# Kernel optimization log

Measured on AMD Instinct MI355X. Metric: run time of the kernel, lower is better.

The kernel has to match this reference:

```python
import jax, jax.numpy as jnp
import numpy as np


def setup_inputs() -> dict:
    key = jax.random.key(0)
    T, B, I, M = 256, 64, 512, 512
    ks = jax.random.split(key, 16)
    kai_i = np.sqrt(2.0 / I)   # kaiming_normal_ fan_in
    kai_m = np.sqrt(2.0 / M)
    return {
        "inputs":   jax.random.normal(ks[0], (T, B, I), jnp.float32),
        "sememe_c": jax.random.normal(ks[1], (T, B, M), jnp.float32),
        "sememe_h": jax.random.normal(ks[2], (T, B, M), jnp.float32),
        "c0":       jax.random.normal(ks[3], (B, M), jnp.float32),
        "h0":       jax.random.normal(ks[4], (B, M), jnp.float32),
        "W_ioux": jax.random.normal(ks[5], (3 * M, I), jnp.float32) * kai_i,
        "b_ioux": jnp.zeros((3 * M,), jnp.float32),
        "W_iouh": jax.random.normal(ks[6], (3 * M, M), jnp.float32) * kai_m,
        "b_iouh": jnp.zeros((3 * M,), jnp.float32),
        "W_ious": jax.random.normal(ks[7], (3 * M, M), jnp.float32) * kai_m,
        "b_ious": jnp.zeros((3 * M,), jnp.float32),
        "W_fx":  jax.random.normal(ks[8],  (M, I), jnp.float32) * kai_i,
        "b_fx":  jnp.zeros((M,), jnp.float32),
        "W_fxs": jax.random.normal(ks[9],  (M, I), jnp.float32) * kai_i,
        "b_fxs": jnp.zeros((M,), jnp.float32),
        "W_fh":  jax.random.normal(ks[10], (M, M), jnp.float32) * kai_m,
        "b_fh":  jnp.zeros((M,), jnp.float32),
        "W_fs":  jax.random.normal(ks[11], (M, M), jnp.float32) * kai_m,
        "b_fs":  jnp.zeros((M,), jnp.float32),
    }


def reference(inputs, sememe_c, sememe_h, c0, h0,
              W_ioux, b_ioux, W_iouh, b_iouh, W_ious, b_ious,
              W_fx, b_fx, W_fxs, b_fxs, W_fh, b_fh, W_fs, b_fs):
    # Precompute all input-side projections with big GEMMs over [T*B, I].
    iou_x = jnp.einsum('tbi,oi->tbo', inputs, W_ioux) + b_ioux   # [T,B,3M]
    fx_all = jnp.einsum('tbi,oi->tbo', inputs, W_fx) + b_fx       # [T,B,M]
    fxs_all = jnp.einsum('tbi,oi->tbo', inputs, W_fxs) + b_fxs    # [T,B,M]

    def step(carry, xs):
        c, h = carry
        iou_x_t, fx_t, fxs_t, sc_t, sh_t = xs
        iou = iou_x_t + h @ W_iouh.T + b_iouh + sh_t @ W_ious.T + b_ious
        i, o, u = jnp.split(iou, 3, axis=1)
        i = jax.nn.sigmoid(i)
        o = jax.nn.sigmoid(o)
        u = jnp.tanh(u)
        f = jax.nn.sigmoid(h @ W_fh.T + b_fh + fx_t)
        f_s = jax.nn.sigmoid(sh_t @ W_fs.T + b_fs + fxs_t)
        c_new = i * u + f * c + f_s * sc_t
        h_new = o * jnp.tanh(c_new)
        return (c_new, h_new), h_new

    (c_T, h_T), output = jax.lax.scan(
        step, (c0, h0), (iou_x, fx_all, fxs_all, sememe_c, sememe_h))
    return output, c_T, h_T
```

## Files before the change

### kernel.cpp

```cpp
#include <hip/hip_runtime.h>
#include <cstdint>
#include <cstddef>


typedef _Float16 half8 __attribute__((ext_vector_type(8)));
typedef _Float16 half4 __attribute__((ext_vector_type(4)));
typedef float    f32x4 __attribute__((ext_vector_type(4)));

#define T_STEPS 256
#define B_DIM   64
#define M_DIM   512
#define KA      1024
#define NA      2560
#define MA      16384
#define NWG_REC 64
#define FLAG_STRIDE 32

__device__ __forceinline__ float sigmoidf_fast(float x) {
    return 1.0f / (1.0f + __expf(-x));
}
__device__ __forceinline__ float tanhf_fast(float x) {
    float e = __expf(2.0f * x);
    return 1.0f - 2.0f / (e + 1.0f);
}


__global__ void conv_xs(const float* __restrict__ inp, const float* __restrict__ sh,
                        _Float16* __restrict__ xs) {
    int idx = blockIdx.x * blockDim.x + threadIdx.x;
    const int total = MA * KA / 8;
    if (idx >= total) return;
    int row = idx >> 7;
    int col = (idx & 127) * 8;
    const float* src = (col < 512) ? (inp + (size_t)row * 512 + col)
                                   : (sh  + (size_t)row * 512 + (col - 512));
    f32x4 a = *(const f32x4*)src;
    f32x4 b = *(const f32x4*)(src + 4);
    half8 o;
    o[0]=(_Float16)a[0]; o[1]=(_Float16)a[1]; o[2]=(_Float16)a[2]; o[3]=(_Float16)a[3];
    o[4]=(_Float16)b[0]; o[5]=(_Float16)b[1]; o[6]=(_Float16)b[2]; o[7]=(_Float16)b[3];
    *(half8*)(xs + (size_t)idx * 8) = o;
}

__global__ void conv_w(const float* __restrict__ W_ioux, const float* __restrict__ W_ious,
                       const float* __restrict__ W_fx,   const float* __restrict__ W_fxs,
                       const float* __restrict__ W_fs,   _Float16* __restrict__ wc) {
    int idx = blockIdx.x * blockDim.x + threadIdx.x;
    const int total = NA * KA / 8;
    if (idx >= total) return;
    int n = idx >> 7;
    int col = (idx & 127) * 8;
    const float* src = nullptr;
    if (col < 512) {
        int k = col;
        src = (n < 1536) ? (W_ioux + (size_t)n * 512 + k)
            : (n < 2048) ? (W_fx   + (size_t)(n - 1536) * 512 + k)
                         : (W_fxs  + (size_t)(n - 2048) * 512 + k);
    } else {
        int k = col - 512;
        if (n < 1536)      src = W_ious + (size_t)n * 512 + k;
        else if (n >= 2048) src = W_fs  + (size_t)(n - 2048) * 512 + k;
    }
    half8 o;
    if (src) {
        f32x4 a = *(const f32x4*)src;
        f32x4 b = *(const f32x4*)(src + 4);
        o[0]=(_Float16)a[0]; o[1]=(_Float16)a[1]; o[2]=(_Float16)a[2]; o[3]=(_Float16)a[3];
        o[4]=(_Float16)b[0]; o[5]=(_Float16)b[1]; o[6]=(_Float16)b[2]; o[7]=(_Float16)b[3];
    } else {
        #pragma unroll
        for (int i = 0; i < 8; ++i) o[i] = (_Float16)0.0f;
    }
    *(half8*)(wc + (size_t)idx * 8) = o;
}

__global__ void conv_wr(const float* __restrict__ W_iouh, const float* __restrict__ W_fh,
                        _Float16* __restrict__ wr) {
    int idx = blockIdx.x * blockDim.x + threadIdx.x;
    const int total = 2048 * 512 / 8;
    if (idx >= total) return;
    int n = idx >> 6;
    int col = (idx & 63) * 8;
    int wgs = n >> 5, loc = n & 31;
    int g = (loc >> 4) * 2 + ((loc >> 3) & 1);
    int m = wgs * 8 + (loc & 7);
    const float* src = (g < 3) ? (W_iouh + ((size_t)(g * 512 + m)) * 512 + col)
                               : (W_fh   + (size_t)m * 512 + col);
    f32x4 a = *(const f32x4*)src;
    f32x4 b = *(const f32x4*)(src + 4);
    half8 o;
    o[0]=(_Float16)a[0]; o[1]=(_Float16)a[1]; o[2]=(_Float16)a[2]; o[3]=(_Float16)a[3];
    o[4]=(_Float16)b[0]; o[5]=(_Float16)b[1]; o[6]=(_Float16)b[2]; o[7]=(_Float16)b[3];
    *(half8*)(wr + (size_t)idx * 8) = o;
}

__global__ void conv_h0(const float* __restrict__ h0, _Float16* __restrict__ hb) {
    int idx = blockIdx.x * blockDim.x + threadIdx.x;
    const int total = B_DIM * M_DIM / 8;
    if (idx >= total) return;
    f32x4 a = *(const f32x4*)(h0 + (size_t)idx * 8);
    f32x4 b = *(const f32x4*)(h0 + (size_t)idx * 8 + 4);
    half8 o;
    o[0]=(_Float16)a[0]; o[1]=(_Float16)a[1]; o[2]=(_Float16)a[2]; o[3]=(_Float16)a[3];
    o[4]=(_Float16)b[0]; o[5]=(_Float16)b[1]; o[6]=(_Float16)b[2]; o[7]=(_Float16)b[3];
    *(half8*)(hb + (size_t)idx * 8) = o;
}


__global__ __launch_bounds__(256, 2)
void gemm_pre(const _Float16* __restrict__ A, const _Float16* __restrict__ W,
              const float* __restrict__ b_ioux, const float* __restrict__ b_iouh,
              const float* __restrict__ b_ious, const float* __restrict__ b_fx,
              const float* __restrict__ b_fh,   const float* __restrict__ b_fxs,
              const float* __restrict__ b_fs,   const float* __restrict__ smc,
              _Float16* __restrict__ pre, _Float16* __restrict__ addc) {
    __shared__ _Float16 As[128 * 64];
    __shared__ _Float16 Bs[128 * 64];

    const int nwg = 2560;
    int orig = blockIdx.x;
    int wgid = (orig & 7) * (nwg >> 3) + (orig >> 3);
    const int bx = wgid & 127;
    const int by = wgid >> 7;
    const int m0 = bx * 128, n0 = by * 128;

    const int tid = threadIdx.x;
    const int wv = tid >> 6, lane = tid & 63;
    const int lr = lane & 15, lq = lane >> 4;
    const int wr = wv >> 1, wc = wv & 1;

    f32x4 acc[4][4];
    #pragma unroll
    for (int i = 0; i < 4; ++i)
        #pragma unroll
        for (int j = 0; j < 4; ++j)
            #pragma unroll
            for (int r = 0; r < 4; ++r) acc[i][j][r] = 0.0f;

    for (int kt = 0; kt < KA / 64; ++kt) {
        const int k0 = kt * 64;
        #pragma unroll
        for (int j = 0; j < 4; ++j) {
            int L = j * 4096 + wv * 1024 + lane * 16;
            int row = L >> 7;
            int colb = (L & 127) ^ ((row & 7) << 4);
            const char* ga = (const char*)(A + (size_t)(m0 + row) * KA + k0) + colb;
            __builtin_amdgcn_global_load_lds(
                (const __attribute__((address_space(1))) void*)ga,
                (__attribute__((address_space(3))) void*)((char*)As + j * 4096 + wv * 1024),
                16, 0, 0);
            const char* gb = (const char*)(W + (size_t)(n0 + row) * KA + k0) + colb;
            __builtin_amdgcn_global_load_lds(
                (const __attribute__((address_space(1))) void*)gb,
                (__attribute__((address_space(3))) void*)((char*)Bs + j * 4096 + wv * 1024),
                16, 0, 0);
        }
        __syncthreads();

        half8 af[4][2], bf[4][2];
        #pragma unroll
        for (int f = 0; f < 4; ++f) {
            #pragma unroll
            for (int kk = 0; kk < 2; ++kk) {
                {
                    int row = wr * 64 + f * 16 + lr;
                    int byt = row * 128 + (((kk * 32 + lq * 8) * 2) ^ ((row & 7) << 4));
                    af[f][kk] = *(const half8*)((const char*)As + byt);
                }
                {
                    int row = wc * 64 + f * 16 + lr;
                    int byt = row * 128 + (((kk * 32 + lq * 8) * 2) ^ ((row & 7) << 4));
                    bf[f][kk] = *(const half8*)((const char*)Bs + byt);
                }
            }
        }
        #pragma unroll
        for (int kk = 0; kk < 2; ++kk)
            #pragma unroll
            for (int fi = 0; fi < 4; ++fi)
                #pragma unroll
                for (int fj = 0; fj < 4; ++fj)
                    acc[fi][fj] = __builtin_amdgcn_mfma_f32_16x16x32_f16(
                        af[fi][kk], bf[fj][kk], acc[fi][fj], 0, 0, 0);
        __syncthreads();
    }

    #pragma unroll
    for (int fi = 0; fi < 4; ++fi) {
        int row0 = m0 + wr * 64 + fi * 16 + lq * 4;
        int tt = row0 >> 6;
        int b  = row0 & 63;
        #pragma unroll
        for (int fj = 0; fj < 4; ++fj) {
            int col = n0 + wc * 64 + fj * 16 + lr;
            f32x4 v = acc[fi][fj];
            if (col < 2048) {
                int g, mm; float bias;
                if (col < 1536) { g = col >> 9; mm = col & 511;
                                  bias = b_ioux[col] + b_iouh[col] + b_ious[col]; }
                else            { g = 3; mm = col - 1536; bias = b_fx[mm] + b_fh[mm]; }
                half4 hv;
                #pragma unroll
                for (int r = 0; r < 4; ++r) hv[r] = (_Float16)(v[r] + bias);
                *(half4*)(pre + ((((size_t)tt * 4 + g) * 512 + mm) * 64 + b)) = hv;
            } else {
                int mm = col - 2048;
                float bias = b_fxs[mm] + b_fs[mm];
                half4 hv;
                #pragma unroll
                for (int r = 0; r < 4; ++r) {
                    float s  = sigmoidf_fast(v[r] + bias);
                    float sc = smc[((size_t)(tt * 64 + b + r)) * 512 + mm];
                    hv[r] = (_Float16)(s * sc);
                }
                *(half4*)(addc + (((size_t)tt * 512 + mm) * 64 + b)) = hv;
            }
        }
    }
}


__global__ __launch_bounds__(256, 1)
void lstm_rec(const _Float16* __restrict__ Wr, const _Float16* __restrict__ pre,
              const _Float16* __restrict__ addc, const float* __restrict__ c0,
              _Float16* __restrict__ hbuf, float* __restrict__ out,
              int* __restrict__ flags) {
    const int wg = blockIdx.x;
    const int tid = threadIdx.x;
    const int wv = tid >> 6, lane = tid & 63;
    const int lr = lane & 15, lq = lane >> 4;
    const int c8 = (lane >> 3) & 1;
    const int m  = wg * 8 + (lane & 7);
    const int b0 = wv * 16 + lq * 4;

    half8 bfr[2][16];
    #pragma unroll
    for (int nt = 0; nt < 2; ++nt)
        #pragma unroll
        for (int kk = 0; kk < 16; ++kk)
            bfr[nt][kk] = *(const half8*)(Wr + ((size_t)(wg * 32 + nt * 16 + lr)) * 512
                                          + kk * 32 + lq * 8);

    float c[4];
    #pragma unroll
    for (int r = 0; r < 4; ++r) c[r] = c0[(size_t)(b0 + r) * 512 + m];

    half4 pv[2], av;
    #pragma unroll
    for (int nt = 0; nt < 2; ++nt) {
        int g = nt * 2 + c8;
        pv[nt] = *(const half4*)(pre + (((size_t)0 * 4 + g) * 512 + m) * 64 + b0);
    }
    av = *(const half4*)(addc + ((size_t)0 * 512 + m) * 64 + b0);

    const int* myflag = flags + lane * FLAG_STRIDE;

    for (int t = 0; t < T_STEPS; ++t) {
        const _Float16* hr = hbuf + (size_t)(t & 1) * B_DIM * M_DIM;
        const _Float16* bp = hr + (size_t)(wv * 16 + lr) * 512 + lq * 8;

        f32x4 acc[2];
        #pragma unroll
        for (int nt = 0; nt < 2; ++nt)
            #pragma unroll
            for (int r = 0; r < 4; ++r) acc[nt][r] = (float)pv[nt][r];
        half4 avc = av;

        if (t + 1 < T_STEPS) {
            #pragma unroll
            for (int nt = 0; nt < 2; ++nt) {
                int g = nt * 2 + c8;
                pv[nt] = *(const half4*)(pre + (((size_t)(t + 1) * 4 + g) * 512 + m) * 64 + b0);
            }
            av = *(const half4*)(addc + ((size_t)(t + 1) * 512 + m) * 64 + b0);
        }

        half8 af[16];
        asm volatile(
            "global_load_dwordx4 %0,  %16, off sc0 sc1\n\t"
            "global_load_dwordx4 %1,  %16, off offset:64 sc0 sc1\n\t"
            "global_load_dwordx4 %2,  %16, off offset:128 sc0 sc1\n\t"
            "global_load_dwordx4 %3,  %16, off offset:192 sc0 sc1\n\t"
            "global_load_dwordx4 %4,  %16, off offset:256 sc0 sc1\n\t"
            "global_load_dwordx4 %5,  %16, off offset:320 sc0 sc1\n\t"
            "global_load_dwordx4 %6,  %16, off offset:384 sc0 sc1\n\t"
            "global_load_dwordx4 %7,  %16, off offset:448 sc0 sc1\n\t"
            "global_load_dwordx4 %8,  %16, off offset:512 sc0 sc1\n\t"
            "global_load_dwordx4 %9,  %16, off offset:576 sc0 sc1\n\t"
            "global_load_dwordx4 %10, %16, off offset:640 sc0 sc1\n\t"
            "global_load_dwordx4 %11, %16, off offset:704 sc0 sc1\n\t"
            "global_load_dwordx4 %12, %16, off offset:768 sc0 sc1\n\t"
            "global_load_dwordx4 %13, %16, off offset:832 sc0 sc1\n\t"
            "global_load_dwordx4 %14, %16, off offset:896 sc0 sc1\n\t"
            "global_load_dwordx4 %15, %16, off offset:960 sc0 sc1\n\t"
            "s_waitcnt vmcnt(0)"
            : "=&v"(af[0]),  "=&v"(af[1]),  "=&v"(af[2]),  "=&v"(af[3]),
              "=&v"(af[4]),  "=&v"(af[5]),  "=&v"(af[6]),  "=&v"(af[7]),
              "=&v"(af[8]),  "=&v"(af[9]),  "=&v"(af[10]), "=&v"(af[11]),
              "=&v"(af[12]), "=&v"(af[13]), "=&v"(af[14]), "=&v"(af[15])
            : "v"(bp)
            : "memory");

        #pragma unroll
        for (int kk = 0; kk < 16; ++kk) {
            acc[0] = __builtin_amdgcn_mfma_f32_16x16x32_f16(af[kk], bfr[0][kk], acc[0], 0, 0, 0);
            acc[1] = __builtin_amdgcn_mfma_f32_16x16x32_f16(af[kk], bfr[1][kk], acc[1], 0, 0, 0);
        }

        float hnew[4];
        #pragma unroll
        for (int r = 0; r < 4; ++r) {
            float raw0 = acc[0][r];
            float raw1 = acc[1][r];
            float s0 = sigmoidf_fast(raw0);
            float v1 = c8 ? sigmoidf_fast(raw1) : tanhf_fast(raw1);
            float sf = __shfl_xor(v1, 8);
            float cn = s0 * v1 + sf * c[r] + (float)avc[r];
            float tc = tanhf_fast(cn);
            float tcx = __shfl_xor(tc, 8);
            if (!c8) c[r] = cn;
            hnew[r] = s0 * tcx;
        }

        if (t == T_STEPS - 1) {
            if (c8) {
                #pragma unroll
                for (int r = 0; r < 4; ++r)
                    out[((size_t)t * B_DIM + b0 + r) * M_DIM + m] = hnew[r];
            }
            size_t base = (size_t)T_STEPS * B_DIM * M_DIM;
            if (!c8) {
                #pragma unroll
                for (int r = 0; r < 4; ++r)
                    out[base + (size_t)(b0 + r) * M_DIM + m] = c[r];
            } else {
                #pragma unroll
                for (int r = 0; r < 4; ++r)
                    out[base + (size_t)B_DIM * M_DIM + (size_t)(b0 + r) * M_DIM + m] = hnew[r];
            }
        } else {
            _Float16* hw = hbuf + (size_t)((t + 1) & 1) * B_DIM * M_DIM;
            if (c8) {
                #pragma unroll
                for (int r = 0; r < 4; ++r) {
                    _Float16 hv = (_Float16)hnew[r];
                    unsigned int u = (unsigned int)__builtin_bit_cast(unsigned short, hv);
                    asm volatile("global_store_short %0, %1, off sc0 sc1"
                                 :: "v"(hw + (size_t)(b0 + r) * M_DIM + m), "v"(u)
                                 : "memory");
                }
            }
            asm volatile("s_waitcnt vmcnt(0)" ::: "memory");
            __syncthreads();
            if (tid == 0) {
                unsigned int fv = (unsigned int)(t + 1);
                asm volatile("global_store_dword %0, %1, off sc0 sc1"
                             :: "v"(flags + wg * FLAG_STRIDE), "v"(fv) : "memory");
            }
            if (c8) {
                #pragma unroll
                for (int r = 0; r < 4; ++r)
                    out[((size_t)t * B_DIM + b0 + r) * M_DIM + m] = hnew[r];
            }
            const int target = t + 1;
            while (true) {
                int v;
                asm volatile("global_load_dword %0, %1, off sc0 sc1\n\t"
                             "s_waitcnt vmcnt(0)"
                             : "=v"(v) : "v"(myflag) : "memory");
                if (__all(v >= target)) break;
                __builtin_amdgcn_s_sleep(1);
            }
        }
    }
}


extern "C" void kernel_launch(void* const* d_in, const int* in_sizes, int n_in,
                              void* d_out, int out_size, void* d_ws, size_t ws_size,
                              hipStream_t stream) {
    const float* inputs  = (const float*)d_in[0];
    const float* smc     = (const float*)d_in[1];
    const float* smh     = (const float*)d_in[2];
    const float* c0      = (const float*)d_in[3];
    const float* h0      = (const float*)d_in[4];
    const float* W_ioux  = (const float*)d_in[5];
    const float* b_ioux  = (const float*)d_in[6];
    const float* W_iouh  = (const float*)d_in[7];
    const float* b_iouh  = (const float*)d_in[8];
    const float* W_ious  = (const float*)d_in[9];
    const float* b_ious  = (const float*)d_in[10];
    const float* W_fx    = (const float*)d_in[11];
    const float* b_fx    = (const float*)d_in[12];
    const float* W_fxs   = (const float*)d_in[13];
    const float* b_fxs   = (const float*)d_in[14];
    const float* W_fh    = (const float*)d_in[15];
    const float* b_fh    = (const float*)d_in[16];
    const float* W_fs    = (const float*)d_in[17];
    const float* b_fs    = (const float*)d_in[18];

    char* ws = (char*)d_ws;
    size_t off = 0;
    auto alloc = [&](size_t bytes) {
        char* p = ws + off;
        off = (off + bytes + 255) & ~(size_t)255;
        return p;
    };
    _Float16* XS   = (_Float16*)alloc((size_t)MA * KA * 2);
    _Float16* Wc   = (_Float16*)alloc((size_t)NA * KA * 2);
    _Float16* Wr   = (_Float16*)alloc((size_t)2048 * 512 * 2);
    _Float16* hb   = (_Float16*)alloc((size_t)2 * B_DIM * M_DIM * 2);
    _Float16* pre  = (_Float16*)alloc((size_t)T_STEPS * 4 * 512 * 64 * 2);
    _Float16* addc = (_Float16*)alloc((size_t)T_STEPS * 512 * 64 * 2);
    int* flags     = (int*)alloc(NWG_REC * FLAG_STRIDE * sizeof(int));
    if (off > ws_size) return;

    hipMemsetAsync(flags, 0, NWG_REC * FLAG_STRIDE * sizeof(int), stream);
    conv_xs <<<MA * KA / 8 / 256, 256, 0, stream>>>(inputs, smh, XS);
    conv_w  <<<NA * KA / 8 / 256, 256, 0, stream>>>(W_ioux, W_ious, W_fx, W_fxs, W_fs, Wc);
    conv_wr <<<2048 * 512 / 8 / 256, 256, 0, stream>>>(W_iouh, W_fh, Wr);
    conv_h0 <<<B_DIM * M_DIM / 8 / 256, 256, 0, stream>>>(h0, hb);
    gemm_pre<<<2560, 256, 0, stream>>>(XS, Wc, b_ioux, b_iouh, b_ious, b_fx, b_fh,
                                       b_fxs, b_fs, smc, pre, addc);
    lstm_rec<<<NWG_REC, 256, 0, stream>>>(Wr, pre, addc, c0, hb, (float*)d_out, flags);
}
```

Measured before the change: 1.325 ms.

## Replace per-step flag barrier with step-tagged h values polled directly

```diff
diff --git a/kernel.cpp b/kernel.cpp
--- a/kernel.cpp
+++ b/kernel.cpp
@@ -6,6 +6,7 @@
 typedef _Float16 half8 __attribute__((ext_vector_type(8)));
 typedef _Float16 half4 __attribute__((ext_vector_type(4)));
 typedef float    f32x4 __attribute__((ext_vector_type(4)));
+typedef unsigned int uint32x4 __attribute__((ext_vector_type(4)));
 
 #define T_STEPS 256
 #define B_DIM   64
@@ -14,7 +15,6 @@
 #define NA      2560
 #define MA      16384
 #define NWG_REC 64
-#define FLAG_STRIDE 32
 
 __device__ __forceinline__ float sigmoidf_fast(float x) {
     return 1.0f / (1.0f + __expf(-x));
@@ -94,16 +94,21 @@
     *(half8*)(wr + (size_t)idx * 8) = o;
 }
 
-__global__ void conv_h0(const float* __restrict__ h0, _Float16* __restrict__ hb) {
+__global__ void conv_h0(const float* __restrict__ h0, unsigned* __restrict__ hb) {
     int idx = blockIdx.x * blockDim.x + threadIdx.x;
     const int total = B_DIM * M_DIM / 8;
     if (idx >= total) return;
     f32x4 a = *(const f32x4*)(h0 + (size_t)idx * 8);
     f32x4 b = *(const f32x4*)(h0 + (size_t)idx * 8 + 4);
-    half8 o;
-    o[0]=(_Float16)a[0]; o[1]=(_Float16)a[1]; o[2]=(_Float16)a[2]; o[3]=(_Float16)a[3];
-    o[4]=(_Float16)b[0]; o[5]=(_Float16)b[1]; o[6]=(_Float16)b[2]; o[7]=(_Float16)b[3];
-    *(half8*)(hb + (size_t)idx * 8) = o;
+    uint32x4 o0, o1;
+    #pragma unroll
+    for (int j = 0; j < 4; ++j) {
+        _Float16 ha = (_Float16)a[j], hb16 = (_Float16)b[j];
+        o0[j] = (unsigned)__builtin_bit_cast(unsigned short, ha);
+        o1[j] = (unsigned)__builtin_bit_cast(unsigned short, hb16);
+    }
+    *(uint32x4*)(hb + (size_t)idx * 8)     = o0;
+    *(uint32x4*)(hb + (size_t)idx * 8 + 4) = o1;
 }
 
 
@@ -220,11 +225,74 @@
 }
 
 
+template<int HALF>
+__device__ __forceinline__ void gather_half(const char* bp, unsigned tagv,
+                                            uint32x4 (&gv)[16]) {
+    while (true) {
+        if constexpr (HALF == 0) {
+            asm volatile(
+                "global_load_dwordx4 %0,  %16, off sc0 sc1\n\t"
+                "global_load_dwordx4 %1,  %16, off offset:16 sc0 sc1\n\t"
+                "global_load_dwordx4 %2,  %16, off offset:128 sc0 sc1\n\t"
+                "global_load_dwordx4 %3,  %16, off offset:144 sc0 sc1\n\t"
+                "global_load_dwordx4 %4,  %16, off offset:256 sc0 sc1\n\t"
+                "global_load_dwordx4 %5,  %16, off offset:272 sc0 sc1\n\t"
+                "global_load_dwordx4 %6,  %16, off offset:384 sc0 sc1\n\t"
+                "global_load_dwordx4 %7,  %16, off offset:400 sc0 sc1\n\t"
+                "global_load_dwordx4 %8,  %16, off offset:512 sc0 sc1\n\t"
+                "global_load_dwordx4 %9,  %16, off offset:528 sc0 sc1\n\t"
+                "global_load_dwordx4 %10, %16, off offset:640 sc0 sc1\n\t"
+                "global_load_dwordx4 %11, %16, off offset:656 sc0 sc1\n\t"
+                "global_load_dwordx4 %12, %16, off offset:768 sc0 sc1\n\t"
+                "global_load_dwordx4 %13, %16, off offset:784 sc0 sc1\n\t"
+                "global_load_dwordx4 %14, %16, off offset:896 sc0 sc1\n\t"
+                "global_load_dwordx4 %15, %16, off offset:912 sc0 sc1\n\t"
+                "s_waitcnt vmcnt(0)"
+                : "=&v"(gv[0]),  "=&v"(gv[1]),  "=&v"(gv[2]),  "=&v"(gv[3]),
+                  "=&v"(gv[4]),  "=&v"(gv[5]),  "=&v"(gv[6]),  "=&v"(gv[7]),
+                  "=&v"(gv[8]),  "=&v"(gv[9]),  "=&v"(gv[10]), "=&v"(gv[11]),
+                  "=&v"(gv[12]), "=&v"(gv[13]), "=&v"(gv[14]), "=&v"(gv[15])
+                : "v"(bp) : "memory");
+        } else {
+            asm volatile(
+                "global_load_dwordx4 %0,  %16, off offset:1024 sc0 sc1\n\t"
+                "global_load_dwordx4 %1,  %16, off offset:1040 sc0 sc1\n\t"
+                "global_load_dwordx4 %2,  %16, off offset:1152 sc0 sc1\n\t"
+                "global_load_dwordx4 %3,  %16, off offset:1168 sc0 sc1\n\t"
+                "global_load_dwordx4 %4,  %16, off offset:1280 sc0 sc1\n\t"
+                "global_load_dwordx4 %5,  %16, off offset:1296 sc0 sc1\n\t"
+                "global_load_dwordx4 %6,  %16, off offset:1408 sc0 sc1\n\t"
+                "global_load_dwordx4 %7,  %16, off offset:1424 sc0 sc1\n\t"
+                "global_load_dwordx4 %8,  %16, off offset:1536 sc0 sc1\n\t"
+                "global_load_dwordx4 %9,  %16, off offset:1552 sc0 sc1\n\t"
+                "global_load_dwordx4 %10, %16, off offset:1664 sc0 sc1\n\t"
+                "global_load_dwordx4 %11, %16, off offset:1680 sc0 sc1\n\t"
+                "global_load_dwordx4 %12, %16, off offset:1792 sc0 sc1\n\t"
+                "global_load_dwordx4 %13, %16, off offset:1808 sc0 sc1\n\t"
+                "global_load_dwordx4 %14, %16, off offset:1920 sc0 sc1\n\t"
+                "global_load_dwordx4 %15, %16, off offset:1936 sc0 sc1\n\t"
+                "s_waitcnt vmcnt(0)"
+                : "=&v"(gv[0]),  "=&v"(gv[1]),  "=&v"(gv[2]),  "=&v"(gv[3]),
+                  "=&v"(gv[4]),  "=&v"(gv[5]),  "=&v"(gv[6]),  "=&v"(gv[7]),
+                  "=&v"(gv[8]),  "=&v"(gv[9]),  "=&v"(gv[10]), "=&v"(gv[11]),
+                  "=&v"(gv[12]), "=&v"(gv[13]), "=&v"(gv[14]), "=&v"(gv[15])
+                : "v"(bp) : "memory");
+        }
+        unsigned bad = 0;
+        #pragma unroll
+        for (int j = 0; j < 16; ++j)
+            #pragma unroll
+            for (int d = 0; d < 4; ++d)
+                bad |= (gv[j][d] >> 16) ^ tagv;
+        if (__all(bad == 0)) return;
+        __builtin_amdgcn_s_sleep(1);
+    }
+}
+
 __global__ __launch_bounds__(256, 1)
 void lstm_rec(const _Float16* __restrict__ Wr, const _Float16* __restrict__ pre,
               const _Float16* __restrict__ addc, const float* __restrict__ c0,
-              _Float16* __restrict__ hbuf, float* __restrict__ out,
-              int* __restrict__ flags) {
+              unsigned* __restrict__ hbuf, float* __restrict__ out) {
     const int wg = blockIdx.x;
     const int tid = threadIdx.x;
     const int wv = tid >> 6, lane = tid & 63;
@@ -253,11 +321,11 @@
     }
     av = *(const half4*)(addc + ((size_t)0 * 512 + m) * 64 + b0);
 
-    const int* myflag = flags + lane * FLAG_STRIDE;
+    const size_t rowoff = ((size_t)(wv * 16 + lr) * 512 + lq * 8) * 4;
 
     for (int t = 0; t < T_STEPS; ++t) {
-        const _Float16* hr = hbuf + (size_t)(t & 1) * B_DIM * M_DIM;
-        const _Float16* bp = hr + (size_t)(wv * 16 + lr) * 512 + lq * 8;
+        const char* bp = (const char*)hbuf + (size_t)(t & 1) * 131072 + rowoff;
+        const unsigned tagv = (unsigned)t;
 
         f32x4 acc[2];
         #pragma unroll
@@ -275,36 +343,32 @@
             av = *(const half4*)(addc + ((size_t)(t + 1) * 512 + m) * 64 + b0);
         }
 
-        half8 af[16];
-        asm volatile(
-            "global_load_dwordx4 %0,  %16, off sc0 sc1\n\t"
-            "global_load_dwordx4 %1,  %16, off offset:64 sc0 sc1\n\t"
-            "global_load_dwordx4 %2,  %16, off offset:128 sc0 sc1\n\t"
-            "global_load_dwordx4 %3,  %16, off offset:192 sc0 sc1\n\t"
-            "global_load_dwordx4 %4,  %16, off offset:256 sc0 sc1\n\t"
-            "global_load_dwordx4 %5,  %16, off offset:320 sc0 sc1\n\t"
-            "global_load_dwordx4 %6,  %16, off offset:384 sc0 sc1\n\t"
-            "global_load_dwordx4 %7,  %16, off offset:448 sc0 sc1\n\t"
-            "global_load_dwordx4 %8,  %16, off offset:512 sc0 sc1\n\t"
-            "global_load_dwordx4 %9,  %16, off offset:576 sc0 sc1\n\t"
-            "global_load_dwordx4 %10, %16, off offset:640 sc0 sc1\n\t"
-            "global_load_dwordx4 %11, %16, off offset:704 sc0 sc1\n\t"
-            "global_load_dwordx4 %12, %16, off offset:768 sc0 sc1\n\t"
-            "global_load_dwordx4 %13, %16, off offset:832 sc0 sc1\n\t"
-            "global_load_dwordx4 %14, %16, off offset:896 sc0 sc1\n\t"
-            "global_load_dwordx4 %15, %16, off offset:960 sc0 sc1\n\t"
-            "s_waitcnt vmcnt(0)"
-            : "=&v"(af[0]),  "=&v"(af[1]),  "=&v"(af[2]),  "=&v"(af[3]),
-              "=&v"(af[4]),  "=&v"(af[5]),  "=&v"(af[6]),  "=&v"(af[7]),
-              "=&v"(af[8]),  "=&v"(af[9]),  "=&v"(af[10]), "=&v"(af[11]),
-              "=&v"(af[12]), "=&v"(af[13]), "=&v"(af[14]), "=&v"(af[15])
-            : "v"(bp)
-            : "memory");
-
-        #pragma unroll
-        for (int kk = 0; kk < 16; ++kk) {
-            acc[0] = __builtin_amdgcn_mfma_f32_16x16x32_f16(af[kk], bfr[0][kk], acc[0], 0, 0, 0);
-            acc[1] = __builtin_amdgcn_mfma_f32_16x16x32_f16(af[kk], bfr[1][kk], acc[1], 0, 0, 0);
+        uint32x4 gv[16];
+        gather_half<0>(bp, tagv, gv);
+        #pragma unroll
+        for (int j2 = 0; j2 < 8; ++j2) {
+            uint32x4 a0 = gv[2 * j2], a1 = gv[2 * j2 + 1];
+            uint32x4 pk;
+            pk[0] = __builtin_amdgcn_perm(a0[1], a0[0], 0x05040100u);
+            pk[1] = __builtin_amdgcn_perm(a0[3], a0[2], 0x05040100u);
+            pk[2] = __builtin_amdgcn_perm(a1[1], a1[0], 0x05040100u);
+            pk[3] = __builtin_amdgcn_perm(a1[3], a1[2], 0x05040100u);
+            half8 afk = __builtin_bit_cast(half8, pk);
+            acc[0] = __builtin_amdgcn_mfma_f32_16x16x32_f16(afk, bfr[0][j2], acc[0], 0, 0, 0);
+            acc[1] = __builtin_amdgcn_mfma_f32_16x16x32_f16(afk, bfr[1][j2], acc[1], 0, 0, 0);
+        }
+        gather_half<1>(bp, tagv, gv);
+        #pragma unroll
+        for (int j2 = 0; j2 < 8; ++j2) {
+            uint32x4 a0 = gv[2 * j2], a1 = gv[2 * j2 + 1];
+            uint32x4 pk;
+            pk[0] = __builtin_amdgcn_perm(a0[1], a0[0], 0x05040100u);
+            pk[1] = __builtin_amdgcn_perm(a0[3], a0[2], 0x05040100u);
+            pk[2] = __builtin_amdgcn_perm(a1[1], a1[0], 0x05040100u);
+            pk[3] = __builtin_amdgcn_perm(a1[3], a1[2], 0x05040100u);
+            half8 afk = __builtin_bit_cast(half8, pk);
+            acc[0] = __builtin_amdgcn_mfma_f32_16x16x32_f16(afk, bfr[0][8 + j2], acc[0], 0, 0, 0);
+            acc[1] = __builtin_amdgcn_mfma_f32_16x16x32_f16(afk, bfr[1][8 + j2], acc[1], 0, 0, 0);
         }
 
         float hnew[4];
@@ -339,37 +403,20 @@
                     out[base + (size_t)B_DIM * M_DIM + (size_t)(b0 + r) * M_DIM + m] = hnew[r];
             }
         } else {
-            _Float16* hw = hbuf + (size_t)((t + 1) & 1) * B_DIM * M_DIM;
+            unsigned* hw = hbuf + (size_t)((t + 1) & 1) * 32768;
+            const unsigned tag1 = (unsigned)(t + 1) << 16;
             if (c8) {
                 #pragma unroll
                 for (int r = 0; r < 4; ++r) {
                     _Float16 hv = (_Float16)hnew[r];
-                    unsigned int u = (unsigned int)__builtin_bit_cast(unsigned short, hv);
-                    asm volatile("global_store_short %0, %1, off sc0 sc1"
-                                 :: "v"(hw + (size_t)(b0 + r) * M_DIM + m), "v"(u)
+                    unsigned u = tag1 | (unsigned)__builtin_bit_cast(unsigned short, hv);
+                    asm volatile("global_store_dword %0, %1, off sc0 sc1"
+                                 :: "v"(hw + (size_t)(b0 + r) * 512 + m), "v"(u)
                                  : "memory");
                 }
-            }
-            asm volatile("s_waitcnt vmcnt(0)" ::: "memory");
-            __syncthreads();
-            if (tid == 0) {
-                unsigned int fv = (unsigned int)(t + 1);
-                asm volatile("global_store_dword %0, %1, off sc0 sc1"
-                             :: "v"(flags + wg * FLAG_STRIDE), "v"(fv) : "memory");
-            }
-            if (c8) {
                 #pragma unroll
                 for (int r = 0; r < 4; ++r)
                     out[((size_t)t * B_DIM + b0 + r) * M_DIM + m] = hnew[r];
-            }
-            const int target = t + 1;
-            while (true) {
-                int v;
-                asm volatile("global_load_dword %0, %1, off sc0 sc1\n\t"
-                             "s_waitcnt vmcnt(0)"
-                             : "=v"(v) : "v"(myflag) : "memory");
-                if (__all(v >= target)) break;
-                __builtin_amdgcn_s_sleep(1);
             }
         }
     }
@@ -409,18 +456,16 @@
     _Float16* XS   = (_Float16*)alloc((size_t)MA * KA * 2);
     _Float16* Wc   = (_Float16*)alloc((size_t)NA * KA * 2);
     _Float16* Wr   = (_Float16*)alloc((size_t)2048 * 512 * 2);
-    _Float16* hb   = (_Float16*)alloc((size_t)2 * B_DIM * M_DIM * 2);
+    unsigned* hb   = (unsigned*)alloc((size_t)2 * B_DIM * M_DIM * 4);
     _Float16* pre  = (_Float16*)alloc((size_t)T_STEPS * 4 * 512 * 64 * 2);
     _Float16* addc = (_Float16*)alloc((size_t)T_STEPS * 512 * 64 * 2);
-    int* flags     = (int*)alloc(NWG_REC * FLAG_STRIDE * sizeof(int));
     if (off > ws_size) return;
 
-    hipMemsetAsync(flags, 0, NWG_REC * FLAG_STRIDE * sizeof(int), stream);
     conv_xs <<<MA * KA / 8 / 256, 256, 0, stream>>>(inputs, smh, XS);
     conv_w  <<<NA * KA / 8 / 256, 256, 0, stream>>>(W_ioux, W_ious, W_fx, W_fxs, W_fs, Wc);
     conv_wr <<<2048 * 512 / 8 / 256, 256, 0, stream>>>(W_iouh, W_fh, Wr);
     conv_h0 <<<B_DIM * M_DIM / 8 / 256, 256, 0, stream>>>(h0, hb);
     gemm_pre<<<2560, 256, 0, stream>>>(XS, Wc, b_ioux, b_iouh, b_ious, b_fx, b_fh,
                                        b_fxs, b_fs, smc, pre, addc);
-    lstm_rec<<<NWG_REC, 256, 0, stream>>>(Wr, pre, addc, c0, hb, (float*)d_out, flags);
-}
+    lstm_rec<<<NWG_REC, 256, 0, stream>>>(Wr, pre, addc, c0, hb, (float*)d_out);
+}
```

After: 2.112 ms. 1.59x slower.

## Replace flag-based grid barrier with step tags embedded in h low bits

Applied to the files above, without the earlier changes.

```diff
diff --git a/kernel.cpp b/kernel.cpp
--- a/kernel.cpp
+++ b/kernel.cpp
@@ -6,6 +6,7 @@
 typedef _Float16 half8 __attribute__((ext_vector_type(8)));
 typedef _Float16 half4 __attribute__((ext_vector_type(4)));
 typedef float    f32x4 __attribute__((ext_vector_type(4)));
+typedef unsigned int uint32x4 __attribute__((ext_vector_type(4)));
 
 #define T_STEPS 256
 #define B_DIM   64
@@ -14,7 +15,6 @@
 #define NA      2560
 #define MA      16384
 #define NWG_REC 64
-#define FLAG_STRIDE 32
 
 __device__ __forceinline__ float sigmoidf_fast(float x) {
     return 1.0f / (1.0f + __expf(-x));
@@ -94,16 +94,25 @@
     *(half8*)(wr + (size_t)idx * 8) = o;
 }
 
-__global__ void conv_h0(const float* __restrict__ h0, _Float16* __restrict__ hb) {
+__global__ void conv_h0(const float* __restrict__ h0, unsigned short* __restrict__ hb) {
     int idx = blockIdx.x * blockDim.x + threadIdx.x;
     const int total = B_DIM * M_DIM / 8;
     if (idx >= total) return;
     f32x4 a = *(const f32x4*)(h0 + (size_t)idx * 8);
     f32x4 b = *(const f32x4*)(h0 + (size_t)idx * 8 + 4);
-    half8 o;
-    o[0]=(_Float16)a[0]; o[1]=(_Float16)a[1]; o[2]=(_Float16)a[2]; o[3]=(_Float16)a[3];
-    o[4]=(_Float16)b[0]; o[5]=(_Float16)b[1]; o[6]=(_Float16)b[2]; o[7]=(_Float16)b[3];
-    *(half8*)(hb + (size_t)idx * 8) = o;
+    unsigned short o[8];
+    #pragma unroll
+    for (int j = 0; j < 4; ++j) {
+        _Float16 ha = (_Float16)a[j], hbv = (_Float16)b[j];
+        o[j]     = (unsigned short)(__builtin_bit_cast(unsigned short, ha)  & 0xFFFCu);
+        o[j + 4] = (unsigned short)(__builtin_bit_cast(unsigned short, hbv) & 0xFFFCu);
+    }
+    uint32x4 pk;
+    pk[0] = o[0] | ((unsigned)o[1] << 16);
+    pk[1] = o[2] | ((unsigned)o[3] << 16);
+    pk[2] = o[4] | ((unsigned)o[5] << 16);
+    pk[3] = o[6] | ((unsigned)o[7] << 16);
+    *(uint32x4*)(hb + (size_t)idx * 8) = pk;
 }
 
 
@@ -223,8 +232,7 @@
 __global__ __launch_bounds__(256, 1)
 void lstm_rec(const _Float16* __restrict__ Wr, const _Float16* __restrict__ pre,
               const _Float16* __restrict__ addc, const float* __restrict__ c0,
-              _Float16* __restrict__ hbuf, float* __restrict__ out,
-              int* __restrict__ flags) {
+              unsigned short* __restrict__ hbuf, float* __restrict__ out) {
     const int wg = blockIdx.x;
     const int tid = threadIdx.x;
     const int wv = tid >> 6, lane = tid & 63;
@@ -253,11 +261,11 @@
     }
     av = *(const half4*)(addc + ((size_t)0 * 512 + m) * 64 + b0);
 
-    const int* myflag = flags + lane * FLAG_STRIDE;
+    const size_t rowoff = ((size_t)(wv * 16 + lr) * 512 + lq * 8) * 2;
 
     for (int t = 0; t < T_STEPS; ++t) {
-        const _Float16* hr = hbuf + (size_t)(t & 1) * B_DIM * M_DIM;
-        const _Float16* bp = hr + (size_t)(wv * 16 + lr) * 512 + lq * 8;
+        const char* bp = (const char*)hbuf + (size_t)(t & 1) * 65536 + rowoff;
+        const unsigned pat = (unsigned)(t & 3) * 0x00010001u;
 
         f32x4 acc[2];
         #pragma unroll
@@ -276,30 +284,42 @@
         }
 
         half8 af[16];
-        asm volatile(
-            "global_load_dwordx4 %0,  %16, off sc0 sc1\n\t"
-            "global_load_dwordx4 %1,  %16, off offset:64 sc0 sc1\n\t"
-            "global_load_dwordx4 %2,  %16, off offset:128 sc0 sc1\n\t"
-            "global_load_dwordx4 %3,  %16, off offset:192 sc0 sc1\n\t"
-            "global_load_dwordx4 %4,  %16, off offset:256 sc0 sc1\n\t"
-            "global_load_dwordx4 %5,  %16, off offset:320 sc0 sc1\n\t"
-            "global_load_dwordx4 %6,  %16, off offset:384 sc0 sc1\n\t"
-            "global_load_dwordx4 %7,  %16, off offset:448 sc0 sc1\n\t"
-            "global_load_dwordx4 %8,  %16, off offset:512 sc0 sc1\n\t"
-            "global_load_dwordx4 %9,  %16, off offset:576 sc0 sc1\n\t"
-            "global_load_dwordx4 %10, %16, off offset:640 sc0 sc1\n\t"
-            "global_load_dwordx4 %11, %16, off offset:704 sc0 sc1\n\t"
-            "global_load_dwordx4 %12, %16, off offset:768 sc0 sc1\n\t"
-            "global_load_dwordx4 %13, %16, off offset:832 sc0 sc1\n\t"
-            "global_load_dwordx4 %14, %16, off offset:896 sc0 sc1\n\t"
-            "global_load_dwordx4 %15, %16, off offset:960 sc0 sc1\n\t"
-            "s_waitcnt vmcnt(0)"
-            : "=&v"(af[0]),  "=&v"(af[1]),  "=&v"(af[2]),  "=&v"(af[3]),
-              "=&v"(af[4]),  "=&v"(af[5]),  "=&v"(af[6]),  "=&v"(af[7]),
-              "=&v"(af[8]),  "=&v"(af[9]),  "=&v"(af[10]), "=&v"(af[11]),
-              "=&v"(af[12]), "=&v"(af[13]), "=&v"(af[14]), "=&v"(af[15])
-            : "v"(bp)
-            : "memory");
+        while (true) {
+            asm volatile(
+                "global_load_dwordx4 %0,  %16, off sc0 sc1\n\t"
+                "global_load_dwordx4 %1,  %16, off offset:64 sc0 sc1\n\t"
+                "global_load_dwordx4 %2,  %16, off offset:128 sc0 sc1\n\t"
+                "global_load_dwordx4 %3,  %16, off offset:192 sc0 sc1\n\t"
+                "global_load_dwordx4 %4,  %16, off offset:256 sc0 sc1\n\t"
+                "global_load_dwordx4 %5,  %16, off offset:320 sc0 sc1\n\t"
+                "global_load_dwordx4 %6,  %16, off offset:384 sc0 sc1\n\t"
+                "global_load_dwordx4 %7,  %16, off offset:448 sc0 sc1\n\t"
+                "global_load_dwordx4 %8,  %16, off offset:512 sc0 sc1\n\t"
+                "global_load_dwordx4 %9,  %16, off offset:576 sc0 sc1\n\t"
+                "global_load_dwordx4 %10, %16, off offset:640 sc0 sc1\n\t"
+                "global_load_dwordx4 %11, %16, off offset:704 sc0 sc1\n\t"
+                "global_load_dwordx4 %12, %16, off offset:768 sc0 sc1\n\t"
+                "global_load_dwordx4 %13, %16, off offset:832 sc0 sc1\n\t"
+                "global_load_dwordx4 %14, %16, off offset:896 sc0 sc1\n\t"
+                "global_load_dwordx4 %15, %16, off offset:960 sc0 sc1\n\t"
+                "s_waitcnt vmcnt(0)"
+                : "=&v"(af[0]),  "=&v"(af[1]),  "=&v"(af[2]),  "=&v"(af[3]),
+                  "=&v"(af[4]),  "=&v"(af[5]),  "=&v"(af[6]),  "=&v"(af[7]),
+                  "=&v"(af[8]),  "=&v"(af[9]),  "=&v"(af[10]), "=&v"(af[11]),
+                  "=&v"(af[12]), "=&v"(af[13]), "=&v"(af[14]), "=&v"(af[15])
+                : "v"(bp)
+                : "memory");
+            unsigned bad = 0;
+            #pragma unroll
+            for (int j = 0; j < 16; ++j) {
+                uint32x4 dv = __builtin_bit_cast(uint32x4, af[j]);
+                #pragma unroll
+                for (int d = 0; d < 4; ++d)
+                    bad |= (dv[d] & 0x00030003u) ^ pat;
+            }
+            if (__all(bad == 0)) break;
+            __builtin_amdgcn_s_sleep(1);
+        }
 
         #pragma unroll
         for (int kk = 0; kk < 16; ++kk) {
@@ -339,37 +359,21 @@
                     out[base + (size_t)B_DIM * M_DIM + (size_t)(b0 + r) * M_DIM + m] = hnew[r];
             }
         } else {
-            _Float16* hw = hbuf + (size_t)((t + 1) & 1) * B_DIM * M_DIM;
+            unsigned short* hw = hbuf + (size_t)((t + 1) & 1) * 32768;
+            const unsigned tag1 = (unsigned)((t + 1) & 3);
             if (c8) {
                 #pragma unroll
                 for (int r = 0; r < 4; ++r) {
                     _Float16 hv = (_Float16)hnew[r];
-                    unsigned int u = (unsigned int)__builtin_bit_cast(unsigned short, hv);
+                    unsigned u = ((unsigned)__builtin_bit_cast(unsigned short, hv)
+                                  & 0xFFFCu) | tag1;
                     asm volatile("global_store_short %0, %1, off sc0 sc1"
-                                 :: "v"(hw + (size_t)(b0 + r) * M_DIM + m), "v"(u)
+                                 :: "v"(hw + (size_t)(b0 + r) * 512 + m), "v"(u)
                                  : "memory");
                 }
-            }
-            asm volatile("s_waitcnt vmcnt(0)" ::: "memory");
-            __syncthreads();
-            if (tid == 0) {
-                unsigned int fv = (unsigned int)(t + 1);
-                asm volatile("global_store_dword %0, %1, off sc0 sc1"
-                             :: "v"(flags + wg * FLAG_STRIDE), "v"(fv) : "memory");
-            }
-            if (c8) {
                 #pragma unroll
                 for (int r = 0; r < 4; ++r)
                     out[((size_t)t * B_DIM + b0 + r) * M_DIM + m] = hnew[r];
-            }
-            const int target = t + 1;
-            while (true) {
-                int v;
-                asm volatile("global_load_dword %0, %1, off sc0 sc1\n\t"
-                             "s_waitcnt vmcnt(0)"
-                             : "=v"(v) : "v"(myflag) : "memory");
-                if (__all(v >= target)) break;
-                __builtin_amdgcn_s_sleep(1);
             }
         }
     }
@@ -409,18 +413,16 @@
     _Float16* XS   = (_Float16*)alloc((size_t)MA * KA * 2);
     _Float16* Wc   = (_Float16*)alloc((size_t)NA * KA * 2);
     _Float16* Wr   = (_Float16*)alloc((size_t)2048 * 512 * 2);
-    _Float16* hb   = (_Float16*)alloc((size_t)2 * B_DIM * M_DIM * 2);
+    unsigned short* hb = (unsigned short*)alloc((size_t)2 * B_DIM * M_DIM * 2);
     _Float16* pre  = (_Float16*)alloc((size_t)T_STEPS * 4 * 512 * 64 * 2);
     _Float16* addc = (_Float16*)alloc((size_t)T_STEPS * 512 * 64 * 2);
-    int* flags     = (int*)alloc(NWG_REC * FLAG_STRIDE * sizeof(int));
     if (off > ws_size) return;
 
-    hipMemsetAsync(flags, 0, NWG_REC * FLAG_STRIDE * sizeof(int), stream);
     conv_xs <<<MA * KA / 8 / 256, 256, 0, stream>>>(inputs, smh, XS);
     conv_w  <<<NA * KA / 8 / 256, 256, 0, stream>>>(W_ioux, W_ious, W_fx, W_fxs, W_fs, Wc);
     conv_wr <<<2048 * 512 / 8 / 256, 256, 0, stream>>>(W_iouh, W_fh, Wr);
     conv_h0 <<<B_DIM * M_DIM / 8 / 256, 256, 0, stream>>>(h0, hb);
     gemm_pre<<<2560, 256, 0, stream>>>(XS, Wc, b_ioux, b_iouh, b_ious, b_fx, b_fh,
                                        b_fxs, b_fs, smc, pre, addc);
-    lstm_rec<<<NWG_REC, 256, 0, stream>>>(Wr, pre, addc, c0, hb, (float*)d_out, flags);
-}
+    lstm_rec<<<NWG_REC, 256, 0, stream>>>(Wr, pre, addc, c0, hb, (float*)d_out);
+}
```

After: 1.892 ms. 42.9% more time.
